# Kernel optimization log

Measured on AMD Instinct MI355X. Metric: run time of the kernel, lower is better.

## Reference

```python
import jax, jax.numpy as jnp
import numpy as np

B, S, D, H, DK, L, DFF, V = 64, 128, 512, 8, 64, 6, 2048, 72
AH = 2          # heads of the internal mask-generating attention encoder (hard-coded n_heads=2)
PRECET = 0.2    # fraction of lowest-attention prefix tokens to mask
NEG = -1e9


def pos_enc(s, d):
    pos = jnp.arange(s, dtype=jnp.float32)[:, None]
    div = jnp.exp(jnp.arange(0, d, 2, dtype=jnp.float32) * (-np.log(10000.0) / d))
    pe = jnp.zeros((s, d), jnp.float32)
    pe = pe.at[:, 0::2].set(jnp.sin(pos * div))
    pe = pe.at[:, 1::2].set(jnp.cos(pos * div))
    return pe


def ln(x, eps=1e-5):  # LayerNorm with default (identity) affine params, as in the source
    m = x.mean(-1, keepdims=True)
    v = ((x - m) ** 2).mean(-1, keepdims=True)
    return (x - m) / jnp.sqrt(v + eps)


def attn_block(x, pad, WQ, WK, WV, WO, heads):
    b, s, _ = x.shape
    dk = WQ.shape[1] // heads
    q = (x @ WQ).reshape(b, s, heads, dk).transpose(0, 2, 1, 3)
    k = (x @ WK).reshape(b, s, heads, dk).transpose(0, 2, 1, 3)
    v = (x @ WV).reshape(b, s, heads, dk).transpose(0, 2, 1, 3)
    scores = jnp.einsum('bhqd,bhkd->bhqk', q, k) / np.sqrt(dk)
    scores = jnp.where(pad[:, None, None, :], NEG, scores)
    attn = jax.nn.softmax(scores, axis=-1)
    ascore = attn.sum(axis=2)                                   # [b, h, s] column sums
    ctx = jnp.einsum('bhqk,bhkd->bqhd', attn, v).reshape(b, s, heads * dk)
    return ln(ctx @ WO + x), attn, ascore


def ffn_block(x, W1, W2):
    return ln(jax.nn.relu(x @ W1) @ W2 + x)


def encode(x, pad, tWQ, tWK, tWV, tFC, tF1, tF2):
    def step(h, p):
        WQ, WK, WV, WO, W1, W2 = p
        h, _, asc = attn_block(h, pad, WQ, WK, WV, WO, H)
        h = ffn_block(h, W1, W2)
        return h, asc.sum(axis=1)                               # sum over heads -> [b, s]
    h, scores = jax.lax.scan(step, x, (tWQ, tWK, tWV, tFC, tF1, tF2))
    return h, scores                                            # scores: [L, b, s]


def creat_mask(col, tokens):
    # col[i, j] == 0 exactly iff token j is pad (softmax of -1e9 underflows to 0).
    b, s = tokens.shape
    iszero = col == 0.0
    has = iszero.any(axis=1)
    j0 = jnp.where(has, jnp.argmax(iszero, axis=1), s)          # first pad position
    kk = jnp.where(has, jnp.ceil(PRECET * j0.astype(jnp.float32)).astype(jnp.int32), 0)
    idx = jnp.arange(s)
    vals = jnp.where(idx[None, :] < j0[:, None], col, jnp.inf)
    ranks = jnp.argsort(jnp.argsort(vals, axis=1), axis=1)      # rank 0 = smallest attention
    keep = (ranks >= kk[:, None]).astype(tokens.dtype)
    return tokens * keep


def pre_head(x, pW1, pb1, pW2, pb2, pW3, pb3):
    x = jax.nn.relu(x @ pW1 + pb1)
    x = jax.nn.relu(x @ pW2 + pb2)
    return x @ pW3 + pb3


def setup_inputs():
    key = jax.random.key(0)
    ks = jax.random.split(key, 18)
    g = lambda k, shp: jax.random.normal(k, shp, jnp.float32) * 0.02
    return {
        'tokens': jax.random.randint(ks[0], (B, S), 0, V, dtype=jnp.int32),
        'emb': g(ks[1], (V, D)),
        'aWQ': g(ks[2], (D, AH * DK)), 'aWK': g(ks[3], (D, AH * DK)), 'aWV': g(ks[4], (D, AH * DK)),
        'aFC': g(ks[5], (AH * DK, D)), 'aF1': g(ks[6], (D, DFF)), 'aF2': g(ks[7], (DFF, D)),
        'tWQ': g(ks[8], (L, D, H * DK)), 'tWK': g(ks[9], (L, D, H * DK)), 'tWV': g(ks[10], (L, D, H * DK)),
        'tFC': g(ks[11], (L, H * DK, D)), 'tF1': g(ks[12], (L, D, DFF)), 'tF2': g(ks[13], (L, DFF, D)),
        'pW1': g(ks[14], (D * S, 1024)), 'pb1': jnp.zeros((1024,), jnp.float32),
        'pW2': g(ks[15], (1024, 512)), 'pb2': jnp.zeros((512,), jnp.float32),
        'pW3': g(ks[16], (512, 128)), 'pb3': jnp.zeros((128,), jnp.float32),
    }


def reference(tokens, emb, aWQ, aWK, aWV, aFC, aF1, aF2,
              tWQ, tWK, tWV, tFC, tF1, tF2,
              pW1, pb1, pW2, pb2, pW3, pb3):
    pe = pos_enc(S, D)[None]
    pad = tokens == 0
    x = emb[tokens] + pe
    # 1-layer / 2-head mask-generating encoder; only its attn matrix is consumed downstream
    _, mattn, _ = attn_block(x, pad, aWQ, aWK, aWV, aFC, AH)
    col = mattn.sum(axis=1).sum(axis=1)                         # heads then queries -> [B, S]
    mtok = creat_mask(col, tokens)
    xm = emb[mtok] + pe
    h, scores = encode(x, pad, tWQ, tWK, tWV, tFC, tF1, tF2)
    hm, _ = encode(xm, mtok == 0, tWQ, tWK, tWV, tFC, tF1, tF2)
    out1 = pre_head(h.reshape(B, -1), pW1, pb1, pW2, pb2, pW3, pb3)
    outm = pre_head(hm.reshape(B, -1), pW1, pb1, pW2, pb2, pW3, pb3)
    return tokens, out1, mtok, outm, scores
```

## Files before the change

kernel.cpp:

```cpp
#include <hip/hip_runtime.h>
#include <hip/hip_bf16.h>
#include <math.h>

using u16 = unsigned short;
using u32 = unsigned int;

constexpr int B   = 64;
constexpr int S   = 128;
constexpr int D   = 512;
constexpr int H   = 8;
constexpr int DK  = 64;
constexpr int L   = 6;
constexpr int DFF = 2048;
constexpr int AH  = 2;
constexpr int BS  = B * S;
constexpr int BS2 = 2 * BS;

constexpr long OUT_TOK    = 0;
constexpr long OUT_OUT1   = 8192;
constexpr long OUT_MTOK   = 16384;
constexpr long OUT_OUTM   = 24576;
constexpr long OUT_SCORES = 32768;

constexpr long OFF_PE   = 0;
constexpr long OFF_ASCL = 65536;
constexpr long OFF_COLP = 851968;
constexpr long OFF_MTOK = 868352;
constexpr long OFF_X    = 876544;
constexpr long OFF_XB   = 9265152;
constexpr long OFF_Y    = 13459456;
constexpr long OFF_QB   = 17653760;
constexpr long OFF_KB   = 21848064;
constexpr long OFF_VB   = 26042368;
constexpr long OFF_TB   = 30236672;
constexpr long OFF_W    = 47013888;
constexpr long WSTRIDE  = 3145728;
constexpr long ASCL_STRIDE = 131072;

typedef __attribute__((ext_vector_type(8))) short bf16x8;
typedef __attribute__((ext_vector_type(4))) float f32x4;

__device__ __forceinline__ float b2f(u16 u) {
    union { u32 i; float f; } v; v.i = ((u32)u) << 16; return v.f;
}
__device__ __forceinline__ u16 f2b(float f) {
    union { float f; u32 i; } v; v.f = f;
    u32 r = v.i + 0x7fffu + ((v.i >> 16) & 1u);
    return (u16)(r >> 16);
}

#define GLOAD_LDS16(g, l) __builtin_amdgcn_global_load_lds(                        \
    (const __attribute__((address_space(1))) u32*)(const void*)(g),               \
    (__attribute__((address_space(3))) u32*)(void*)(l), 16, 0, 0)

__global__ void pe_kernel(float* __restrict__ pe) {
    int idx = blockIdx.x * 256 + threadIdx.x;
    if (idx >= S * (D / 2)) return;
    int s = idx >> 8;
    int i = idx & 255;
    const float CPE = (float)(-9.210340371976184 / 512.0);
    float div = expf((float)(2 * i) * CPE);
    float ang = (float)s * div;
    pe[(long)s * D + 2 * i]     = sinf(ang);
    pe[(long)s * D + 2 * i + 1] = cosf(ang);
}

__global__ void embed_dual(const int* __restrict__ toks, const float* __restrict__ emb,
                           const float* __restrict__ pe, float* x,
                           u16* __restrict__ xb) {
    int i8 = blockIdx.x * 256 + threadIdx.x;
    if (i8 >= BS * D / 8) return;
    int row = i8 >> 6;
    int c8  = i8 & 63;
    int s   = row & (S - 1);
    int t   = toks[row];
    float4 e0 = *(const float4*)(emb + (long)t * D + c8 * 8);
    float4 e1 = *(const float4*)(emb + (long)t * D + c8 * 8 + 4);
    float4 p0 = *(const float4*)(pe + (long)s * D + c8 * 8);
    float4 p1 = *(const float4*)(pe + (long)s * D + c8 * 8 + 4);
    float4 o0, o1;
    o0.x = e0.x + p0.x; o0.y = e0.y + p0.y; o0.z = e0.z + p0.z; o0.w = e0.w + p0.w;
    o1.x = e1.x + p1.x; o1.y = e1.y + p1.y; o1.z = e1.z + p1.z; o1.w = e1.w + p1.w;
    if (x) {
        *(float4*)(x + (long)i8 * 8)     = o0;
        *(float4*)(x + (long)i8 * 8 + 4) = o1;
    }
    u16 u[8] = {f2b(o0.x), f2b(o0.y), f2b(o0.z), f2b(o0.w), f2b(o1.x), f2b(o1.y), f2b(o1.z), f2b(o1.w)};
    *(uint4*)(xb + (long)i8 * 8) = *(uint4*)u;
}

__global__ __launch_bounds__(256)
void wconv_all(const float* __restrict__ tWQ, const float* __restrict__ tWK,
               const float* __restrict__ tWV, const float* __restrict__ tFC,
               const float* __restrict__ tF1, const float* __restrict__ tF2,
               u16* __restrict__ wAll) {
    __shared__ float t[32][33];
    const int lyr = blockIdx.x / 3072;
    const int bid = blockIdx.x % 3072;
    u16* base = wAll + (long)lyr * WSTRIDE;
    const float* src; u16* dst; int KK, NN, tk, tn;
    if (bid < 1024) {
        int which = bid >> 8, tt = bid & 255;
        src = (which == 0 ? tWQ : which == 1 ? tWK : which == 2 ? tWV : tFC) + (long)lyr * D * D;
        dst = base + (long)which * 262144;
        KK = 512; NN = 512; tk = tt >> 4; tn = tt & 15;
    } else if (bid < 2048) {
        int tt = bid - 1024;
        src = tF1 + (long)lyr * D * DFF; dst = base + 1048576;
        KK = 512; NN = 2048; tk = tt >> 6; tn = tt & 63;
    } else {
        int tt = bid - 2048;
        src = tF2 + (long)lyr * DFF * D; dst = base + 2097152;
        KK = 2048; NN = 512; tk = tt >> 4; tn = tt & 15;
    }
    int ty = threadIdx.x >> 5, tx = threadIdx.x & 31;
    #pragma unroll
    for (int i = 0; i < 4; i++)
        t[ty + i * 8][tx] = src[(long)(tk * 32 + ty + i * 8) * NN + tn * 32 + tx];
    __syncthreads();
    #pragma unroll
    for (int i = 0; i < 4; i++)
        dst[(long)(tn * 32 + ty + i * 8) * KK + tk * 32 + tx] = f2b(t[tx][ty + i * 8]);
}

template<int EPI, int OUTB>
__device__ __forceinline__ void gemm_core(
        const u16* __restrict__ A, const u16* __restrict__ Wt,
        float* C, u16* Cb, const u16* __restrict__ X,
        int M, int N, int K, int m0, int n0) {
    __shared__ u16 As[2][128 * 32];
    __shared__ u16 Bs[2][128 * 32];
    const int tid = threadIdx.x;
    const int w = tid >> 6, l = tid & 63;
    const int wr = (w >> 1) * 64, wc = (w & 1) * 64;
    f32x4 acc[4][4];
    #pragma unroll
    for (int i = 0; i < 4; i++)
        #pragma unroll
        for (int j = 0; j < 4; j++) { f32x4 z = {0.f, 0.f, 0.f, 0.f}; acc[i][j] = z; }

    const int srow = w * 32 + (l >> 2);
    const int scol = (l & 3) * 8;
    const u16* gA = A + (long)(m0 + srow) * K + scol;
    const u16* gB = Wt + (long)(n0 + srow) * K + scol;

    for (int k0 = 0; k0 < K; k0 += 64) {
        #pragma unroll
        for (int p = 0; p < 2; p++) {
            GLOAD_LDS16(gA + k0 + p * 32,               As[p] + w * 1024);
            GLOAD_LDS16(gA + (long)16 * K + k0 + p * 32, As[p] + w * 1024 + 512);
            GLOAD_LDS16(gB + k0 + p * 32,               Bs[p] + w * 1024);
            GLOAD_LDS16(gB + (long)16 * K + k0 + p * 32, Bs[p] + w * 1024 + 512);
        }
        __syncthreads();
        #pragma unroll
        for (int p = 0; p < 2; p++) {
            bf16x8 aF[4], bF[4];
            #pragma unroll
            for (int mi = 0; mi < 4; mi++)
                aF[mi] = *(const bf16x8*)(As[p] + (wr + mi * 16 + (l & 15)) * 32 + (l >> 4) * 8);
            #pragma unroll
            for (int ni = 0; ni < 4; ni++)
                bF[ni] = *(const bf16x8*)(Bs[p] + (wc + ni * 16 + (l & 15)) * 32 + (l >> 4) * 8);
            #pragma unroll
            for (int mi = 0; mi < 4; mi++)
                #pragma unroll
                for (int ni = 0; ni < 4; ni++)
                    acc[mi][ni] = __builtin_amdgcn_mfma_f32_16x16x32_bf16(aF[mi], bF[ni], acc[mi][ni], 0, 0, 0);
        }
        __syncthreads();
    }

    #pragma unroll
    for (int mi = 0; mi < 4; mi++) {
        #pragma unroll
        for (int ni = 0; ni < 4; ni++) {
            const int col = n0 + wc + ni * 16 + (l & 15);
            #pragma unroll
            for (int r = 0; r < 4; r++) {
                const int row = m0 + wr + mi * 16 + (l >> 4) * 4 + r;
                const long idx = (long)row * N + col;
                float v = acc[mi][ni][r];
                if (EPI == 3) v += b2f(X[idx]);
                if (EPI == 2) v = fmaxf(v, 0.0f);
                if (OUTB) Cb[idx] = f2b(v);
                else      C[idx]  = v;
            }
        }
    }
}

__global__ __launch_bounds__(256)
void gemm_qkv_b(const u16* __restrict__ A, const u16* wq, const u16* wk, const u16* wv,
                u16* qb, u16* kb, u16* vb, int M, int N, int K) {
    const u16* Wt = blockIdx.z == 0 ? wq : blockIdx.z == 1 ? wk : wv;
    u16* Cb       = blockIdx.z == 0 ? qb : blockIdx.z == 1 ? kb : vb;
    gemm_core<0, 1>(A, Wt, nullptr, Cb, nullptr, M, N, K, blockIdx.x * 128, blockIdx.y * 128);
}
__global__ __launch_bounds__(256)
void gemm_resid_b(const u16* __restrict__ A, const u16* __restrict__ Wt,
                  u16* Yb, const u16* __restrict__ X, int M, int N, int K) {
    gemm_core<3, 1>(A, Wt, nullptr, Yb, X, M, N, K, blockIdx.x * 128, blockIdx.y * 128);
}
__global__ __launch_bounds__(256)
void gemm_relu_b(const u16* __restrict__ A, const u16* __restrict__ Wt,
                 u16* Cb, int M, int N, int K) {
    gemm_core<2, 1>(A, Wt, nullptr, Cb, nullptr, M, N, K, blockIdx.x * 128, blockIdx.y * 128);
}

template<int EPI>
__global__ __launch_bounds__(256)
void gemm64(const float* __restrict__ A, const float* __restrict__ W,
            float* C, const float* X, int M, int N, int K) {
    __shared__ float As[32][68];
    __shared__ float Ws[32][64];
    const int m0 = blockIdx.x * 64, n0 = blockIdx.y * 64;
    const int tid  = threadIdx.x;
    const int tr   = tid >> 4, tc = tid & 15;
    const int arow = tid >> 3, acg = tid & 7;
    const int wrow = tid >> 4, wcg = tid & 15;
    float acc[4][4] = {};
    for (int k0 = 0; k0 < K; k0 += 32) {
        float4 a0 = *(const float4*)(A + (long)(m0 + arow) * K + k0 + acg * 4);
        float4 a1 = *(const float4*)(A + (long)(m0 + arow + 32) * K + k0 + acg * 4);
        float4 w0 = *(const float4*)(W + (long)(k0 + wrow) * N + n0 + wcg * 4);
        float4 w1 = *(const float4*)(W + (long)(k0 + wrow + 16) * N + n0 + wcg * 4);
        As[acg * 4 + 0][arow] = a0.x; As[acg * 4 + 1][arow] = a0.y;
        As[acg * 4 + 2][arow] = a0.z; As[acg * 4 + 3][arow] = a0.w;
        As[acg * 4 + 0][arow + 32] = a1.x; As[acg * 4 + 1][arow + 32] = a1.y;
        As[acg * 4 + 2][arow + 32] = a1.z; As[acg * 4 + 3][arow + 32] = a1.w;
        *(float4*)&Ws[wrow][wcg * 4]      = w0;
        *(float4*)&Ws[wrow + 16][wcg * 4] = w1;
        __syncthreads();
        #pragma unroll
        for (int kk = 0; kk < 32; kk++) {
            float4 av = *(const float4*)&As[kk][tr * 4];
            float4 bv = *(const float4*)&Ws[kk][tc * 4];
            acc[0][0] += av.x * bv.x; acc[0][1] += av.x * bv.y; acc[0][2] += av.x * bv.z; acc[0][3] += av.x * bv.w;
            acc[1][0] += av.y * bv.x; acc[1][1] += av.y * bv.y; acc[1][2] += av.y * bv.z; acc[1][3] += av.y * bv.w;
            acc[2][0] += av.z * bv.x; acc[2][1] += av.z * bv.y; acc[2][2] += av.z * bv.z; acc[2][3] += av.z * bv.w;
            acc[3][0] += av.w * bv.x; acc[3][1] += av.w * bv.y; acc[3][2] += av.w * bv.z; acc[3][3] += av.w * bv.w;
        }
        __syncthreads();
    }
    #pragma unroll
    for (int i = 0; i < 4; i++) {
        int row = m0 + tr * 4 + i;
        #pragma unroll
        for (int j = 0; j < 4; j++) {
            int col = n0 + tc * 4 + j;
            long idx = (long)row * N + col;
            float v = acc[i][j];
            if (EPI == 1) v += X[idx];
            if (EPI == 3 || EPI == 4) v += X[col];
            if (EPI == 2 || EPI == 4) v = fmaxf(v, 0.0f);
            C[idx] = v;
        }
    }
}

__global__ __launch_bounds__(256)
void gemm64_qkv(const float* __restrict__ A,
                const float* __restrict__ WQ, const float* __restrict__ WK, const float* __restrict__ WV,
                float* q, float* k, float* v, int M, int N, int K) {
    __shared__ float As[32][68];
    __shared__ float Ws[32][64];
    const float* W = (blockIdx.z == 0) ? WQ : (blockIdx.z == 1) ? WK : WV;
    float*       C = (blockIdx.z == 0) ? q  : (blockIdx.z == 1) ? k  : v;
    const int m0 = blockIdx.x * 64, n0 = blockIdx.y * 64;
    const int tid  = threadIdx.x;
    const int tr   = tid >> 4, tc = tid & 15;
    const int arow = tid >> 3, acg = tid & 7;
    const int wrow = tid >> 4, wcg = tid & 15;
    float acc[4][4] = {};
    for (int k0 = 0; k0 < K; k0 += 32) {
        float4 a0 = *(const float4*)(A + (long)(m0 + arow) * K + k0 + acg * 4);
        float4 a1 = *(const float4*)(A + (long)(m0 + arow + 32) * K + k0 + acg * 4);
        float4 w0 = *(const float4*)(W + (long)(k0 + wrow) * N + n0 + wcg * 4);
        float4 w1 = *(const float4*)(W + (long)(k0 + wrow + 16) * N + n0 + wcg * 4);
        As[acg * 4 + 0][arow] = a0.x; As[acg * 4 + 1][arow] = a0.y;
        As[acg * 4 + 2][arow] = a0.z; As[acg * 4 + 3][arow] = a0.w;
        As[acg * 4 + 0][arow + 32] = a1.x; As[acg * 4 + 1][arow + 32] = a1.y;
        As[acg * 4 + 2][arow + 32] = a1.z; As[acg * 4 + 3][arow + 32] = a1.w;
        *(float4*)&Ws[wrow][wcg * 4]      = w0;
        *(float4*)&Ws[wrow + 16][wcg * 4] = w1;
        __syncthreads();
        #pragma unroll
        for (int kk = 0; kk < 32; kk++) {
            float4 av = *(const float4*)&As[kk][tr * 4];
            float4 bv = *(const float4*)&Ws[kk][tc * 4];
            acc[0][0] += av.x * bv.x; acc[0][1] += av.x * bv.y; acc[0][2] += av.x * bv.z; acc[0][3] += av.x * bv.w;
            acc[1][0] += av.y * bv.x; acc[1][1] += av.y * bv.y; acc[1][2] += av.y * bv.z; acc[1][3] += av.y * bv.w;
            acc[2][0] += av.z * bv.x; acc[2][1] += av.z * bv.y; acc[2][2] += av.z * bv.z; acc[2][3] += av.z * bv.w;
            acc[3][0] += av.w * bv.x; acc[3][1] += av.w * bv.y; acc[3][2] += av.w * bv.z; acc[3][3] += av.w * bv.w;
        }
        __syncthreads();
    }
    #pragma unroll
    for (int i = 0; i < 4; i++)
        #pragma unroll
        for (int j = 0; j < 4; j++)
            C[(long)(m0 + tr * 4 + i) * N + n0 + tc * 4 + j] = acc[i][j];
}

__global__ __launch_bounds__(256)
void gemm_ph1(const u16* __restrict__ Ah, const u16* __restrict__ Ahm,
              const float* __restrict__ W, float* __restrict__ P, int KC) {
    constexpr int N = 1024, K = 65536;
    __shared__ u16 As[128 * 32];
    __shared__ u16 Bs[128 * 32];
    const int n0 = blockIdx.x * 128;
    const int kbeg = blockIdx.y * KC;
    const int tid = threadIdx.x;
    const int w = tid >> 6, l = tid & 63;
    const int wr = w * 32;
    const int nl = tid >> 1, seg = tid & 1;
    const u16* aptr = (nl < 64 ? Ah + (long)nl * K : Ahm + (long)(nl - 64) * K) + seg * 16;
    const float* wcol = W + n0 + nl;

    f32x4 acc[2][8];
    #pragma unroll
    for (int mi = 0; mi < 2; mi++)
        #pragma unroll
        for (int ni = 0; ni < 8; ni++) { f32x4 z = {0.f, 0.f, 0.f, 0.f}; acc[mi][ni] = z; }

    for (int ks = 0; ks < KC; ks += 32) {
        const int k0 = kbeg + ks;
        uint4 a0 = *(const uint4*)(aptr + k0);
        uint4 a1 = *(const uint4*)(aptr + k0 + 8);
        float wv[16];
        #pragma unroll
        for (int j = 0; j < 16; j++)
            wv[j] = wcol[(long)(k0 + seg * 16 + j) * N];
        __syncthreads();
        *(uint4*)(As + nl * 32 + seg * 16)     = a0;
        *(uint4*)(As + nl * 32 + seg * 16 + 8) = a1;
        u32 pk[8];
        #pragma unroll
        for (int j = 0; j < 8; j++)
            pk[j] = (u32)f2b(wv[2 * j]) | ((u32)f2b(wv[2 * j + 1]) << 16);
        *(uint4*)(Bs + nl * 32 + seg * 16)     = *(uint4*)&pk[0];
        *(uint4*)(Bs + nl * 32 + seg * 16 + 8) = *(uint4*)&pk[4];
        __syncthreads();
        bf16x8 aF0 = *(const bf16x8*)(As + (wr + (l & 15)) * 32 + (l >> 4) * 8);
        bf16x8 aF1 = *(const bf16x8*)(As + (wr + 16 + (l & 15)) * 32 + (l >> 4) * 8);
        #pragma unroll
        for (int ni = 0; ni < 8; ni++) {
            bf16x8 bF = *(const bf16x8*)(Bs + (ni * 16 + (l & 15)) * 32 + (l >> 4) * 8);
            acc[0][ni] = __builtin_amdgcn_mfma_f32_16x16x32_bf16(aF0, bF, acc[0][ni], 0, 0, 0);
            acc[1][ni] = __builtin_amdgcn_mfma_f32_16x16x32_bf16(aF1, bF, acc[1][ni], 0, 0, 0);
        }
    }
    float* Pz = P + (long)blockIdx.y * 128 * N;
    #pragma unroll
    for (int mi = 0; mi < 2; mi++)
        #pragma unroll
        for (int ni = 0; ni < 8; ni++) {
            const int col = n0 + ni * 16 + (l & 15);
            #pragma unroll
            for (int r = 0; r < 4; r++)
                Pz[(long)(wr + mi * 16 + (l >> 4) * 4 + r) * N + col] = acc[mi][ni][r];
        }
}

__global__ __launch_bounds__(128)
void attn_kernel(const float* __restrict__ Q, const float* __restrict__ K,
                 const int* __restrict__ toks, float* __restrict__ colsum, int Hn) {
    __shared__ float sc[S][129];
    __shared__ float KV[S][DK];
    __shared__ int   padS[S];
    const int b = blockIdx.x / Hn;
    const int h = blockIdx.x % Hn;
    const int stride = Hn * DK;
    const int tid = threadIdx.x;

    for (int idx = tid; idx < S * DK; idx += 128) {
        int r = idx >> 6, c = idx & 63;
        KV[r][c] = K[(long)(b * S + r) * stride + h * DK + c];
    }
    padS[tid] = (toks[b * S + tid] == 0) ? 1 : 0;
    float qreg[DK];
    {
        const float* qp = Q + (long)(b * S + tid) * stride + h * DK;
        #pragma unroll
        for (int i = 0; i < 16; i++) {
            float4 t4 = *(const float4*)(qp + i * 4);
            qreg[i * 4 + 0] = t4.x; qreg[i * 4 + 1] = t4.y;
            qreg[i * 4 + 2] = t4.z; qreg[i * 4 + 3] = t4.w;
        }
    }
    __syncthreads();
    for (int k = 0; k < S; k++) {
        float s = 0.0f;
        #pragma unroll
        for (int d4 = 0; d4 < 16; d4++) {
            float4 kv = *(const float4*)&KV[k][d4 * 4];
            s += qreg[d4 * 4 + 0] * kv.x + qreg[d4 * 4 + 1] * kv.y
               + qreg[d4 * 4 + 2] * kv.z + qreg[d4 * 4 + 3] * kv.w;
        }
        sc[tid][k] = padS[k] ? -1e9f : (s * 0.125f);
    }
    float mx = -INFINITY;
    for (int k = 0; k < S; k++) mx = fmaxf(mx, sc[tid][k]);
    float sum = 0.0f;
    for (int k = 0; k < S; k++) { float e = expf(sc[tid][k] - mx); sc[tid][k] = e; sum += e; }
    for (int k = 0; k < S; k++) sc[tid][k] = sc[tid][k] / sum;
    __syncthreads();
    {
        double a = 0.0;
        for (int q2 = 0; q2 < S; q2++) a += (double)sc[q2][tid];
        colsum[(long)(b * Hn + h) * S + tid] = (float)a;
    }
}

__global__ __launch_bounds__(256)
void attn_mfma_kernel(u16* qb, const u16* __restrict__ kb, const u16* __restrict__ vb,
                      const int* __restrict__ toks, const int* __restrict__ mtok,
                      float* __restrict__ colsum) {
    __shared__ u16 pool[18432];
    __shared__ u16 Vt[64 * 136];
    __shared__ float colsLds[4][128];
    __shared__ u32 padF[128];
    u16* Qs = pool;
    u16* Ks = pool + 9216;
    u16* Ps = pool;

    const int gb = blockIdx.x >> 3, h = blockIdx.x & 7;
    const int tid = threadIdx.x;
    const int w = tid >> 6, l = tid & 63;
    const long base = (long)gb * S * D + h * 64;
    const int* tsrc = (gb < B) ? (toks + (long)gb * S) : (mtok + (long)(gb - B) * S);

    for (int j = tid; j < 1024; j += 256) {
        int r = j >> 3, c = j & 7;
        uint4 uq = *(const uint4*)(qb + base + (long)r * D + c * 8);
        uint4 uk = *(const uint4*)(kb + base + (long)r * D + c * 8);
        uint4 uv = *(const uint4*)(vb + base + (long)r * D + c * 8);
        *(uint4*)(Qs + r * 72 + c * 8) = uq;
        *(uint4*)(Ks + r * 72 + c * 8) = uk;
        u16 vv[8]; *(uint4*)vv = uv;
        #pragma unroll
        for (int t = 0; t < 8; t++) Vt[(c * 8 + t) * 136 + r] = vv[t];
    }
    if (tid < 128) padF[tid] = (tsrc[tid] == 0) ? 1u : 0u;
    __syncthreads();

    const int rowB = w * 32;
    f32x4 acc[2][8];
    #pragma unroll
    for (int mi = 0; mi < 2; mi++)
        #pragma unroll
        for (int ni = 0; ni < 8; ni++) { f32x4 z = {0.f, 0.f, 0.f, 0.f}; acc[mi][ni] = z; }
    #pragma unroll
    for (int ks = 0; ks < 2; ks++) {
        bf16x8 a0 = *(const bf16x8*)(Qs + (rowB + (l & 15)) * 72 + ks * 32 + (l >> 4) * 8);
        bf16x8 a1 = *(const bf16x8*)(Qs + (rowB + 16 + (l & 15)) * 72 + ks * 32 + (l >> 4) * 8);
        #pragma unroll
        for (int ni = 0; ni < 8; ni++) {
            bf16x8 bv = *(const bf16x8*)(Ks + (ni * 16 + (l & 15)) * 72 + ks * 32 + (l >> 4) * 8);
            acc[0][ni] = __builtin_amdgcn_mfma_f32_16x16x32_bf16(a0, bv, acc[0][ni], 0, 0, 0);
            acc[1][ni] = __builtin_amdgcn_mfma_f32_16x16x32_bf16(a1, bv, acc[1][ni], 0, 0, 0);
        }
    }
    float pf[8];
    #pragma unroll
    for (int ni = 0; ni < 8; ni++) pf[ni] = padF[ni * 16 + (l & 15)] ? 1.0f : 0.0f;
    #pragma unroll
    for (int mi = 0; mi < 2; mi++)
        #pragma unroll
        for (int ni = 0; ni < 8; ni++)
            #pragma unroll
            for (int r = 0; r < 4; r++) {
                float v = acc[mi][ni][r] * 0.125f;
                acc[mi][ni][r] = (pf[ni] != 0.0f) ? -1e9f : v;
            }
    #pragma unroll
    for (int mi = 0; mi < 2; mi++)
        #pragma unroll
        for (int r = 0; r < 4; r++) {
            float m = -INFINITY;
            #pragma unroll
            for (int ni = 0; ni < 8; ni++) m = fmaxf(m, acc[mi][ni][r]);
            m = fmaxf(m, __shfl_xor(m, 1)); m = fmaxf(m, __shfl_xor(m, 2));
            m = fmaxf(m, __shfl_xor(m, 4)); m = fmaxf(m, __shfl_xor(m, 8));
            float s = 0.0f;
            #pragma unroll
            for (int ni = 0; ni < 8; ni++) { float e = expf(acc[mi][ni][r] - m); acc[mi][ni][r] = e; s += e; }
            s += __shfl_xor(s, 1); s += __shfl_xor(s, 2);
            s += __shfl_xor(s, 4); s += __shfl_xor(s, 8);
            float inv = 1.0f / s;
            #pragma unroll
            for (int ni = 0; ni < 8; ni++) acc[mi][ni][r] *= inv;
        }
    float cs[8];
    #pragma unroll
    for (int ni = 0; ni < 8; ni++) {
        float s = 0.0f;
        #pragma unroll
        for (int mi = 0; mi < 2; mi++)
            #pragma unroll
            for (int r = 0; r < 4; r++) s += acc[mi][ni][r];
        s += __shfl_xor(s, 16); s += __shfl_xor(s, 32);
        cs[ni] = s;
    }
    __syncthreads();
    if (l < 16)
        #pragma unroll
        for (int ni = 0; ni < 8; ni++) colsLds[w][ni * 16 + l] = cs[ni];
    #pragma unroll
    for (int mi = 0; mi < 2; mi++)
        #pragma unroll
        for (int ni = 0; ni < 8; ni++)
            #pragma unroll
            for (int r = 0; r < 4; r++)
                Ps[(rowB + mi * 16 + (l >> 4) * 4 + r) * 136 + ni * 16 + (l & 15)] =
                    f2b(acc[mi][ni][r]);
    __syncthreads();
    if (tid < 128) {
        float s = colsLds[0][tid] + colsLds[1][tid] + colsLds[2][tid] + colsLds[3][tid];
        colsum[((long)gb * H + h) * S + tid] = s;
    }
    f32x4 o[2][4];
    #pragma unroll
    for (int mi = 0; mi < 2; mi++)
        #pragma unroll
        for (int n = 0; n < 4; n++) { f32x4 z = {0.f, 0.f, 0.f, 0.f}; o[mi][n] = z; }
    #pragma unroll
    for (int ks = 0; ks < 4; ks++) {
        bf16x8 p0 = *(const bf16x8*)(Ps + (rowB + (l & 15)) * 136 + ks * 32 + (l >> 4) * 8);
        bf16x8 p1 = *(const bf16x8*)(Ps + (rowB + 16 + (l & 15)) * 136 + ks * 32 + (l >> 4) * 8);
        #pragma unroll
        for (int n = 0; n < 4; n++) {
            bf16x8 bv = *(const bf16x8*)(Vt + (n * 16 + (l & 15)) * 136 + ks * 32 + (l >> 4) * 8);
            o[0][n] = __builtin_amdgcn_mfma_f32_16x16x32_bf16(p0, bv, o[0][n], 0, 0, 0);
            o[1][n] = __builtin_amdgcn_mfma_f32_16x16x32_bf16(p1, bv, o[1][n], 0, 0, 0);
        }
    }
    #pragma unroll
    for (int mi = 0; mi < 2; mi++)
        #pragma unroll
        for (int n = 0; n < 4; n++) {
            const int col = n * 16 + (l & 15);
            #pragma unroll
            for (int r = 0; r < 4; r++) {
                const int row = rowB + mi * 16 + (l >> 4) * 4 + r;
                qb[base + (long)row * D + col] = f2b(o[mi][n][r]);
            }
        }
}

__global__ __launch_bounds__(128)
void creat_mask_kernel(const float* __restrict__ colpart, const int* __restrict__ toks,
                       int* __restrict__ mtok, float* __restrict__ out) {
    __shared__ float colS[S];
    __shared__ int   j0s, kks;
    const int b = blockIdx.x, j = threadIdx.x;
    float c = colpart[(long)(b * AH + 0) * S + j] + colpart[(long)(b * AH + 1) * S + j];
    colS[j] = c;
    int tk = toks[b * S + j];
    __syncthreads();
    if (j == 0) {
        int j0 = S;
        for (int i = 0; i < S; i++) if (colS[i] == 0.0f) { j0 = i; break; }
        int kk = (j0 < S) ? (int)ceilf(0.2f * (float)j0) : 0;
        j0s = j0; kks = kk;
    }
    __syncthreads();
    const int j0 = j0s, kk = kks;
    float vj = (j < j0) ? colS[j] : INFINITY;
    int rank = 0;
    for (int i = 0; i < S; i++) {
        float vi = (i < j0) ? colS[i] : INFINITY;
        if (vi < vj || (vi == vj && i < j)) rank++;
    }
    int mt = (rank >= kk) ? tk : 0;
    mtok[b * S + j] = mt;
    out[OUT_TOK + b * S + j]  = (float)tk;
    out[OUT_MTOK + b * S + j] = (float)mt;
}

__global__ __launch_bounds__(256)
void ln_kernel(const u16* __restrict__ y, u16* __restrict__ xb) {
    const int row  = blockIdx.x * 4 + (threadIdx.x >> 6);
    const int lane = threadIdx.x & 63;
    const u16* r = y + (long)row * D;
    uint4 u = *(const uint4*)(r + lane * 8);
    u32 uu[4] = {u.x, u.y, u.z, u.w};
    float v[8];
    #pragma unroll
    for (int t = 0; t < 4; t++) {
        v[t * 2]     = b2f((u16)(uu[t] & 0xffffu));
        v[t * 2 + 1] = b2f((u16)(uu[t] >> 16));
    }
    float s = 0.0f, q = 0.0f;
    #pragma unroll
    for (int t = 0; t < 8; t++) { s += v[t]; q += v[t] * v[t]; }
    #pragma unroll
    for (int off = 32; off; off >>= 1) { s += __shfl_xor(s, off); q += __shfl_xor(q, off); }
    float m   = s * (1.0f / 512.0f);
    float var = q * (1.0f / 512.0f) - m * m;
    float inv = 1.0f / sqrtf(var + 1e-5f);
    u16 o[8];
    #pragma unroll
    for (int t = 0; t < 8; t++) o[t] = f2b((v[t] - m) * inv);
    *(uint4*)(xb + (long)row * D + lane * 8) = *(uint4*)o;
}

__global__ void score_all_kernel(const float* __restrict__ ascl, float* __restrict__ out) {
    int idx = blockIdx.x * 256 + threadIdx.x;
    if (idx >= L * B * S) return;
    int l   = idx / (B * S);
    int rem = idx - l * (B * S);
    int b = rem >> 7, j = rem & 127;
    const float* p = ascl + (long)l * ASCL_STRIDE + (long)b * H * S + j;
    float s = 0.0f;
    #pragma unroll
    for (int h = 0; h < H; h++) s += p[(long)h * S];
    out[OUT_SCORES + idx] = s;
}

__global__ void reduce1_kernel(const float* __restrict__ parts, const float* __restrict__ b1,
                               float* __restrict__ o) {
    int idx = blockIdx.x * 256 + threadIdx.x;
    if (idx >= 128 * 1024) return;
    float s = 0.0f;
    for (int z = 0; z < 64; z++) s += parts[(long)z * 128 * 1024 + idx];
    s += b1[idx & 1023];
    o[idx] = fmaxf(s, 0.0f);
}

__global__ void pack_out_kernel(const float* __restrict__ ph3, float* __restrict__ out) {
    int idx = blockIdx.x * 256 + threadIdx.x;
    if (idx >= 128 * 128) return;
    int row = idx >> 7, col = idx & 127;
    long base = (row < 64) ? (OUT_OUT1 + (long)row * 128) : (OUT_OUTM + (long)(row - 64) * 128);
    out[base + col] = ph3[idx];
}

extern "C" void kernel_launch(void* const* d_in, const int* in_sizes, int n_in,
                              void* d_out, int out_size, void* d_ws, size_t ws_size,
                              hipStream_t stream) {
    const int*   toks = (const int*)d_in[0];
    const float* emb  = (const float*)d_in[1];
    const float* aWQ  = (const float*)d_in[2];
    const float* aWK  = (const float*)d_in[3];
    const float* tWQ  = (const float*)d_in[8];
    const float* tWK  = (const float*)d_in[9];
    const float* tWV  = (const float*)d_in[10];
    const float* tFC  = (const float*)d_in[11];
    const float* tF1  = (const float*)d_in[12];
    const float* tF2  = (const float*)d_in[13];
    const float* pW1  = (const float*)d_in[14];
    const float* pb1  = (const float*)d_in[15];
    const float* pW2  = (const float*)d_in[16];
    const float* pb2  = (const float*)d_in[17];
    const float* pW3  = (const float*)d_in[18];
    const float* pb3  = (const float*)d_in[19];
    float* out = (float*)d_out;

    float* ws   = (float*)d_ws;
    float* pe   = ws + OFF_PE;
    float* ascl = ws + OFF_ASCL;
    float* colp = ws + OFF_COLP;
    int*   mtok = (int*)(ws + OFF_MTOK);
    float* x    = ws + OFF_X;
    u16*   xb   = (u16*)(ws + OFF_XB);
    u16*   yb   = (u16*)(ws + OFF_Y);
    u16*   qb   = (u16*)(ws + OFF_QB);
    u16*   kb   = (u16*)(ws + OFF_KB);
    u16*   vb   = (u16*)(ws + OFF_VB);
    u16*   tb   = (u16*)(ws + OFF_TB);
    u16*   wAll = (u16*)(ws + OFF_W);

    float* maq   = ws + OFF_TB;
    float* mak   = maq + (long)BS * 128;
    float* parts = ws + OFF_TB;
    float* ph1o  = parts + 8388608;
    float* ph2o  = ph1o + 131072;
    float* ph3o  = ph2o + 65536;

    pe_kernel<<<128, 256, 0, stream>>>(pe);
    wconv_all<<<6 * 3072, 256, 0, stream>>>(tWQ, tWK, tWV, tFC, tF1, tF2, wAll);
    embed_dual<<<2048, 256, 0, stream>>>(toks, emb, pe, x, xb);

    gemm64_qkv<<<dim3(BS / 64, 2, 2), 256, 0, stream>>>(
        x, aWQ, aWK, nullptr, maq, mak, nullptr, BS, AH * DK, D);
    attn_kernel<<<B * AH, 128, 0, stream>>>(maq, mak, toks, colp, AH);
    creat_mask_kernel<<<B, 128, 0, stream>>>(colp, toks, mtok, out);
    embed_dual<<<2048, 256, 0, stream>>>(mtok, emb, pe, nullptr, xb + (long)BS * D);

    for (int l = 0; l < L; l++) {
        const u16* wq = wAll + (long)l * WSTRIDE;
        const u16* wk = wq + 262144;
        const u16* wv = wq + 524288;
        const u16* wo = wq + 786432;
        const u16* w1 = wq + 1048576;
        const u16* w2 = wq + 2097152;
        gemm_qkv_b<<<dim3(BS2 / 128, D / 128, 3), 256, 0, stream>>>(
            xb, wq, wk, wv, qb, kb, vb, BS2, D, D);
        attn_mfma_kernel<<<2 * B * H, 256, 0, stream>>>(
            qb, kb, vb, toks, mtok, ascl + (long)l * ASCL_STRIDE);
        gemm_resid_b<<<dim3(BS2 / 128, D / 128), 256, 0, stream>>>(qb, wo, yb, xb, BS2, D, D);
        ln_kernel<<<BS2 / 4, 256, 0, stream>>>(yb, xb);
        gemm_relu_b<<<dim3(BS2 / 128, DFF / 128), 256, 0, stream>>>(xb, w1, tb, BS2, DFF, D);
        gemm_resid_b<<<dim3(BS2 / 128, D / 128), 256, 0, stream>>>(tb, w2, yb, xb, BS2, D, DFF);
        ln_kernel<<<BS2 / 4, 256, 0, stream>>>(yb, xb);
    }
    score_all_kernel<<<192, 256, 0, stream>>>(ascl, out);

    gemm_ph1<<<dim3(8, 64), 256, 0, stream>>>(xb, xb + (long)BS * D, pW1, parts, 1024);
    reduce1_kernel<<<512, 256, 0, stream>>>(parts, pb1, ph1o);
    gemm64<4><<<dim3(2, 8), 256, 0, stream>>>(ph1o, pW2, ph2o, pb2, 128, 512, 1024);
    gemm64<3><<<dim3(2, 2), 256, 0, stream>>>(ph2o, pW3, ph3o, pb3, 128, 128, 512);
    pack_out_kernel<<<64, 256, 0, stream>>>(ph3o, out);
}
```

Before: 1.472 ms.

## Use 256x128 tiles with 512-thread blocks for QKV and FFN1 GEMMs

Adds a new GEMM core using a 256x128 output tile per 512-thread block (8 waves, each computing 64x64). It loads two 32-wide K slices into LDS per sync round via direct global-to-LDS loads, and the QKV and ReLU FFN1 GEMMs now use it. The aim is more operand reuse per block and fewer barriers per K step. In exchange the grid holds half as many blocks, and LDS staging is not double-buffered across iterations, so load latency may be exposed.

```diff
diff --git a/kernel.cpp b/kernel.cpp
--- a/kernel.cpp
+++ b/kernel.cpp
@@ -190,22 +190,86 @@
     }
 }
 
-__global__ __launch_bounds__(256)
+template<int EPI>
+__device__ __forceinline__ void gemm_core256(
+        const u16* __restrict__ A, const u16* __restrict__ Wt, u16* __restrict__ Cb,
+        int M, int N, int K, int m0, int n0) {
+    __shared__ u16 As[2][256 * 32];
+    __shared__ u16 Bs[2][128 * 32];
+    const int tid = threadIdx.x;
+    const int w = tid >> 6, l = tid & 63;
+    const int wr = (w >> 1) * 64, wc = (w & 1) * 64;
+    f32x4 acc[4][4];
+    #pragma unroll
+    for (int i = 0; i < 4; i++)
+        #pragma unroll
+        for (int j = 0; j < 4; j++) { f32x4 z = {0.f, 0.f, 0.f, 0.f}; acc[i][j] = z; }
+
+    const int arow = w * 32 + (l >> 2);
+    const int brow = w * 16 + (l >> 2);
+    const int scol = (l & 3) * 8;
+    const u16* gA = A + (long)(m0 + arow) * K + scol;
+    const u16* gB = Wt + (long)(n0 + brow) * K + scol;
+
+    for (int k0 = 0; k0 < K; k0 += 64) {
+        #pragma unroll
+        for (int p = 0; p < 2; p++) {
+            GLOAD_LDS16(gA + k0 + p * 32,               As[p] + w * 1024);
+            GLOAD_LDS16(gA + (long)16 * K + k0 + p * 32, As[p] + w * 1024 + 512);
+            GLOAD_LDS16(gB + k0 + p * 32,               Bs[p] + w * 512);
+        }
+        __syncthreads();
+        #pragma unroll
+        for (int p = 0; p < 2; p++) {
+            bf16x8 aF[4], bF[4];
+            #pragma unroll
+            for (int mi = 0; mi < 4; mi++)
+                aF[mi] = *(const bf16x8*)(As[p] + (wr + mi * 16 + (l & 15)) * 32 + (l >> 4) * 8);
+            #pragma unroll
+            for (int ni = 0; ni < 4; ni++)
+                bF[ni] = *(const bf16x8*)(Bs[p] + (wc + ni * 16 + (l & 15)) * 32 + (l >> 4) * 8);
+            #pragma unroll
+            for (int mi = 0; mi < 4; mi++)
+                #pragma unroll
+                for (int ni = 0; ni < 4; ni++)
+                    acc[mi][ni] = __builtin_amdgcn_mfma_f32_16x16x32_bf16(aF[mi], bF[ni], acc[mi][ni], 0, 0, 0);
+        }
+        __syncthreads();
+    }
+
+    #pragma unroll
+    for (int mi = 0; mi < 4; mi++) {
+        #pragma unroll
+        for (int ni = 0; ni < 4; ni++) {
+            const int col = n0 + wc + ni * 16 + (l & 15);
+            #pragma unroll
+            for (int r = 0; r < 4; r++) {
+                const int row = m0 + wr + mi * 16 + (l >> 4) * 4 + r;
+                const long idx = (long)row * N + col;
+                float v = acc[mi][ni][r];
+                if (EPI == 2) v = fmaxf(v, 0.0f);
+                Cb[idx] = f2b(v);
+            }
+        }
+    }
+}
+
+__global__ __launch_bounds__(512)
 void gemm_qkv_b(const u16* __restrict__ A, const u16* wq, const u16* wk, const u16* wv,
                 u16* qb, u16* kb, u16* vb, int M, int N, int K) {
     const u16* Wt = blockIdx.z == 0 ? wq : blockIdx.z == 1 ? wk : wv;
     u16* Cb       = blockIdx.z == 0 ? qb : blockIdx.z == 1 ? kb : vb;
-    gemm_core<0, 1>(A, Wt, nullptr, Cb, nullptr, M, N, K, blockIdx.x * 128, blockIdx.y * 128);
+    gemm_core256<0>(A, Wt, Cb, M, N, K, blockIdx.x * 256, blockIdx.y * 128);
+}
+__global__ __launch_bounds__(512)
+void gemm_relu_b(const u16* __restrict__ A, const u16* __restrict__ Wt,
+                 u16* Cb, int M, int N, int K) {
+    gemm_core256<2>(A, Wt, Cb, M, N, K, blockIdx.x * 256, blockIdx.y * 128);
 }
 __global__ __launch_bounds__(256)
 void gemm_resid_b(const u16* __restrict__ A, const u16* __restrict__ Wt,
                   u16* Yb, const u16* __restrict__ X, int M, int N, int K) {
     gemm_core<3, 1>(A, Wt, nullptr, Yb, X, M, N, K, blockIdx.x * 128, blockIdx.y * 128);
-}
-__global__ __launch_bounds__(256)
-void gemm_relu_b(const u16* __restrict__ A, const u16* __restrict__ Wt,
-                 u16* Cb, int M, int N, int K) {
-    gemm_core<2, 1>(A, Wt, nullptr, Cb, nullptr, M, N, K, blockIdx.x * 128, blockIdx.y * 128);
 }
 
 template<int EPI>
@@ -696,13 +760,13 @@
         const u16* wo = wq + 786432;
         const u16* w1 = wq + 1048576;
         const u16* w2 = wq + 2097152;
-        gemm_qkv_b<<<dim3(BS2 / 128, D / 128, 3), 256, 0, stream>>>(
+        gemm_qkv_b<<<dim3(BS2 / 256, D / 128, 3), 512, 0, stream>>>(
             xb, wq, wk, wv, qb, kb, vb, BS2, D, D);
         attn_mfma_kernel<<<2 * B * H, 256, 0, stream>>>(
             qb, kb, vb, toks, mtok, ascl + (long)l * ASCL_STRIDE);
         gemm_resid_b<<<dim3(BS2 / 128, D / 128), 256, 0, stream>>>(qb, wo, yb, xb, BS2, D, D);
         ln_kernel<<<BS2 / 4, 256, 0, stream>>>(yb, xb);
-        gemm_relu_b<<<dim3(BS2 / 128, DFF / 128), 256, 0, stream>>>(xb, w1, tb, BS2, DFF, D);
+        gemm_relu_b<<<dim3(BS2 / 256, DFF / 128), 512, 0, stream>>>(xb, w1, tb, BS2, DFF, D);
         gemm_resid_b<<<dim3(BS2 / 128, D / 128), 256, 0, stream>>>(tb, w2, yb, xb, BS2, D, DFF);
         ln_kernel<<<BS2 / 4, 256, 0, stream>>>(yb, xb);
     }
```

Result: no change. 1.449 ms (median of 2 runs) (-1.5%).
